# Kernel optimization log

Hardware: AMD Instinct MI355X
Metric: run time of the kernel (lower is better)

Reference implementation:

```python
import jax, jax.numpy as jnp
import numpy as np

B, N, C, H, K = 8, 1024, 768, 12, 16


def setup_inputs() -> dict:
    key = jax.random.key(0)
    ks = jax.random.split(key, 5)
    s = 0.02
    return {
        "query": jax.random.normal(ks[0], (B, N, C), jnp.float32),
        "in_proj_weight": jax.random.normal(ks[1], (3 * C, C), jnp.float32) * s,
        "in_proj_bias": jax.random.normal(ks[2], (3 * C,), jnp.float32) * s,
        "out_proj_weight": jax.random.normal(ks[3], (C, C), jnp.float32) * s,
        "out_proj_bias": jax.random.normal(ks[4], (C,), jnp.float32) * s,
        "num_heads": H,
        "k": K,
    }


def reference(query, in_proj_weight, in_proj_bias, out_proj_weight, out_proj_bias, num_heads, k):
    b, n, c = query.shape
    hd = c // num_heads
    scale = hd ** (-0.5)
    # fused QKV projection: F.linear(x, W, b) == x @ W.T + b
    qkv = query @ in_proj_weight.T + in_proj_bias  # [B,N,3C]
    qkv = qkv.reshape(b, n, 3, num_heads, hd).transpose(2, 0, 3, 1, 4)  # [3,B,H,N,hd]
    q, kk, v = qkv[0], qkv[1], qkv[2]
    attn = jnp.einsum("bhqd,bhkd->bhqk", q, kk) * scale
    attn = jax.nn.softmax(attn, axis=-1)  # [B,H,N,N]
    kk_ = min(k, attn.shape[-1])
    vals, idx = jax.lax.top_k(attn, kk_)  # [B,H,N,k]
    bi = jnp.arange(b)[:, None, None, None]
    hi = jnp.arange(num_heads)[None, :, None, None]
    ni = jnp.arange(n)[None, None, :, None]
    topk_attn = jnp.zeros_like(attn).at[bi, hi, ni, idx].set(vals)
    den = jnp.clip(topk_attn.sum(axis=-1, keepdims=True), 1e-6, None)
    topk_attn = topk_attn / den
    out = jnp.einsum("bhqk,bhkd->bhqd", topk_attn, v)  # [B,H,N,hd]
    out = out.transpose(0, 2, 1, 3).reshape(b, n, c)
    out = out @ out_proj_weight.T + out_proj_bias
    return out, topk_attn
```

## Files before the change

kernel.cpp:

```cpp
#include <hip/hip_runtime.h>
#include <float.h>
#include <math.h>

#define B_ 8
#define N_ 1024
#define C_ 768
#define H_ 12
#define HD_ 64
#define BH_ (B_*H_)

typedef __attribute__((ext_vector_type(8))) short bf16x8;
typedef __attribute__((ext_vector_type(4))) float f32x4;

__device__ __forceinline__ unsigned long long makekey(float v, int idx) {
    unsigned int b = __float_as_uint(v);
    unsigned int o = (b & 0x80000000u) ? ~b : (b | 0x80000000u);
    return ((unsigned long long)o << 32) | (unsigned int)(1023 - idx);
}
__device__ __forceinline__ float keyval(unsigned long long k) {
    unsigned int ordv = (unsigned int)(k >> 32);
    unsigned int fb = (ordv & 0x80000000u) ? (ordv & 0x7FFFFFFFu) : ~ordv;
    return __uint_as_float(fb);
}
__device__ __forceinline__ unsigned short f2bf(float f) {
    unsigned int u = __float_as_uint(f);
    return (unsigned short)((u + 0x7FFFu + ((u >> 16) & 1u)) >> 16);
}

template<int MM, int NN, int KD, int MODE>
__global__ void __launch_bounds__(256)
gemm_k(const float* __restrict__ A, const float* __restrict__ W,
       const float* __restrict__ bias, float* __restrict__ out)
{
    __shared__ float As[2][16][132];
    __shared__ float Bs[2][16][132];
    const int tid = threadIdx.x;
    constexpr int NBLK = NN / 128;
    constexpr int NWG = (MM / 128) * NBLK;
    const int eff = (blockIdx.x & 7) * (NWG / 8) + (blockIdx.x >> 3);
    const int bm = eff / NBLK;
    const int bn = eff % NBLK;
    const int m0 = bm * 128, n0 = bn * 128;
    const int ty = tid >> 4, tx = tid & 15;
    const int ar = tid >> 2;
    const int ac = (tid & 3) << 2;

    float acc[8][8];
#pragma unroll
    for (int i = 0; i < 8; ++i)
#pragma unroll
        for (int j = 0; j < 8; ++j) acc[i][j] = 0.f;

    const float* A0 = A + (size_t)(m0 + ar) * KD + ac;
    const float* A1 = A + (size_t)(m0 + ar + 64) * KD + ac;
    const float* W0 = W + (size_t)(n0 + ar) * KD + ac;
    const float* W1 = W + (size_t)(n0 + ar + 64) * KD + ac;

    float4 pa0 = *(const float4*)A0;
    float4 pa1 = *(const float4*)A1;
    float4 pb0 = *(const float4*)W0;
    float4 pb1 = *(const float4*)W1;

    As[0][ac+0][ar]    = pa0.x; As[0][ac+1][ar]    = pa0.y; As[0][ac+2][ar]    = pa0.z; As[0][ac+3][ar]    = pa0.w;
    As[0][ac+0][ar+64] = pa1.x; As[0][ac+1][ar+64] = pa1.y; As[0][ac+2][ar+64] = pa1.z; As[0][ac+3][ar+64] = pa1.w;
    Bs[0][ac+0][ar]    = pb0.x; Bs[0][ac+1][ar]    = pb0.y; Bs[0][ac+2][ar]    = pb0.z; Bs[0][ac+3][ar]    = pb0.w;
    Bs[0][ac+0][ar+64] = pb1.x; Bs[0][ac+1][ar+64] = pb1.y; Bs[0][ac+2][ar+64] = pb1.z; Bs[0][ac+3][ar+64] = pb1.w;
    __syncthreads();

    int cur = 0;
    for (int k0 = 0; k0 < KD; k0 += 16) {
        const bool more = (k0 + 16 < KD);
        if (more) {
            pa0 = *(const float4*)(A0 + k0 + 16);
            pa1 = *(const float4*)(A1 + k0 + 16);
            pb0 = *(const float4*)(W0 + k0 + 16);
            pb1 = *(const float4*)(W1 + k0 + 16);
        }
        const float (*Ac)[132] = As[cur];
        const float (*Bc)[132] = Bs[cur];
#pragma unroll
        for (int kk = 0; kk < 16; ++kk) {
            float4 a0v = *(const float4*)&Ac[kk][ty * 4];
            float4 a1v = *(const float4*)&Ac[kk][64 + ty * 4];
            float4 b0v = *(const float4*)&Bc[kk][tx * 4];
            float4 b1v = *(const float4*)&Bc[kk][64 + tx * 4];
            float av[8] = {a0v.x,a0v.y,a0v.z,a0v.w, a1v.x,a1v.y,a1v.z,a1v.w};
            float bv[8] = {b0v.x,b0v.y,b0v.z,b0v.w, b1v.x,b1v.y,b1v.z,b1v.w};
#pragma unroll
            for (int i = 0; i < 8; ++i)
#pragma unroll
                for (int j = 0; j < 8; ++j)
                    acc[i][j] = fmaf(av[i], bv[j], acc[i][j]);
        }
        if (more) {
            const int nxt = cur ^ 1;
            As[nxt][ac+0][ar]    = pa0.x; As[nxt][ac+1][ar]    = pa0.y; As[nxt][ac+2][ar]    = pa0.z; As[nxt][ac+3][ar]    = pa0.w;
            As[nxt][ac+0][ar+64] = pa1.x; As[nxt][ac+1][ar+64] = pa1.y; As[nxt][ac+2][ar+64] = pa1.z; As[nxt][ac+3][ar+64] = pa1.w;
            Bs[nxt][ac+0][ar]    = pb0.x; Bs[nxt][ac+1][ar]    = pb0.y; Bs[nxt][ac+2][ar]    = pb0.z; Bs[nxt][ac+3][ar]    = pb0.w;
            Bs[nxt][ac+0][ar+64] = pb1.x; Bs[nxt][ac+1][ar+64] = pb1.y; Bs[nxt][ac+2][ar+64] = pb1.z; Bs[nxt][ac+3][ar+64] = pb1.w;
            __syncthreads();
            cur = nxt;
        }
    }

#pragma unroll
    for (int gi = 0; gi < 2; ++gi)
#pragma unroll
    for (int i = 0; i < 4; ++i) {
        const int m = m0 + gi * 64 + ty * 4 + i;
        const int ai = gi * 4 + i;
#pragma unroll
        for (int gj = 0; gj < 2; ++gj) {
            const int o = n0 + gj * 64 + tx * 4;
            const int aj = gj * 4;
            float4 bv4 = *(const float4*)(bias + o);
            float4 v;
            v.x = acc[ai][aj+0] + bv4.x;
            v.y = acc[ai][aj+1] + bv4.y;
            v.z = acc[ai][aj+2] + bv4.z;
            v.w = acc[ai][aj+3] + bv4.w;
            if (MODE == 0) {
                *(float4*)(out + (size_t)m * NN + o) = v;
            } else {
                const int which = o / 768;
                const int r = o - which * 768;
                const int hh = r >> 6;
                const int dd = r & 63;
                const int bh = (m >> 10) * H_ + hh;
                const int nn = m & 1023;
                if (which == 1) {
                    float* dst = out + (size_t)BH_ * N_ * HD_
                               + ((size_t)bh * HD_ + dd) * N_ + nn;
                    dst[0]      = v.x;
                    dst[N_]     = v.y;
                    dst[2 * N_] = v.z;
                    dst[3 * N_] = v.w;
                } else {
                    float* dst = out + ((size_t)bh * N_ + nn) * HD_ + dd;
                    *(float4*)dst = v;
                }
            }
        }
    }
}

template<int MM, int NN, int MODE>
__global__ void __launch_bounds__(256)
gemm_bf_k(const float* __restrict__ A, const float* __restrict__ W,
          const float* __restrict__ bias, float* __restrict__ out)
{
    __shared__ unsigned short Asb[128][40];
    __shared__ unsigned short Bsb[128][40];
    const int tid = threadIdx.x;
    constexpr int NBLK = NN / 128;
    constexpr int NWG = (MM / 128) * NBLK;
    const int eff = (blockIdx.x & 7) * (NWG / 8) + (blockIdx.x >> 3);
    const int bm = eff / NBLK;
    const int bn = eff % NBLK;
    const int m0 = bm * 128, n0 = bn * 128;
    const int lane = tid & 63;
    const int w = tid >> 6;
    const int wm = (w >> 1) << 6;
    const int wn = (w & 1) << 6;

    f32x4 acc[4][4];
#pragma unroll
    for (int i = 0; i < 4; ++i)
#pragma unroll
        for (int j = 0; j < 4; ++j) acc[i][j] = (f32x4){0.f, 0.f, 0.f, 0.f};

    const int srow = tid >> 1;
    const int sks  = (tid & 1) << 4;
    const float* ga = A + (size_t)(m0 + srow) * 768 + sks;
    const float* gw = W + (size_t)(n0 + srow) * 768 + sks;

    for (int k0 = 0; k0 < 768; k0 += 32) {
        __syncthreads();
        {
            float4 f0 = *(const float4*)(ga + k0 + 0);
            float4 f1 = *(const float4*)(ga + k0 + 4);
            float4 f2 = *(const float4*)(ga + k0 + 8);
            float4 f3 = *(const float4*)(ga + k0 + 12);
            unsigned short* d = &Asb[srow][sks];
            d[0]=f2bf(f0.x);  d[1]=f2bf(f0.y);  d[2]=f2bf(f0.z);  d[3]=f2bf(f0.w);
            d[4]=f2bf(f1.x);  d[5]=f2bf(f1.y);  d[6]=f2bf(f1.z);  d[7]=f2bf(f1.w);
            d[8]=f2bf(f2.x);  d[9]=f2bf(f2.y);  d[10]=f2bf(f2.z); d[11]=f2bf(f2.w);
            d[12]=f2bf(f3.x); d[13]=f2bf(f3.y); d[14]=f2bf(f3.z); d[15]=f2bf(f3.w);
            f0 = *(const float4*)(gw + k0 + 0);
            f1 = *(const float4*)(gw + k0 + 4);
            f2 = *(const float4*)(gw + k0 + 8);
            f3 = *(const float4*)(gw + k0 + 12);
            unsigned short* e = &Bsb[srow][sks];
            e[0]=f2bf(f0.x);  e[1]=f2bf(f0.y);  e[2]=f2bf(f0.z);  e[3]=f2bf(f0.w);
            e[4]=f2bf(f1.x);  e[5]=f2bf(f1.y);  e[6]=f2bf(f1.z);  e[7]=f2bf(f1.w);
            e[8]=f2bf(f2.x);  e[9]=f2bf(f2.y);  e[10]=f2bf(f2.z); e[11]=f2bf(f2.w);
            e[12]=f2bf(f3.x); e[13]=f2bf(f3.y); e[14]=f2bf(f3.z); e[15]=f2bf(f3.w);
        }
        __syncthreads();

        bf16x8 af[4], bf[4];
        const int fr = lane & 15;
        const int fk = (lane >> 4) << 3;
#pragma unroll
        for (int fi = 0; fi < 4; ++fi)
            af[fi] = *(const bf16x8*)&Asb[wm + (fi << 4) + fr][fk];
#pragma unroll
        for (int fj = 0; fj < 4; ++fj)
            bf[fj] = *(const bf16x8*)&Bsb[wn + (fj << 4) + fr][fk];
#pragma unroll
        for (int fi = 0; fi < 4; ++fi)
#pragma unroll
            for (int fj = 0; fj < 4; ++fj)
                acc[fi][fj] = __builtin_amdgcn_mfma_f32_16x16x32_bf16(af[fi], bf[fj], acc[fi][fj], 0, 0, 0);
    }

    const int cr = (lane >> 4) << 2;
    const int cc = lane & 15;
#pragma unroll
    for (int fj = 0; fj < 4; ++fj) {
        const int col = n0 + wn + (fj << 4) + cc;
        const float bb = bias[col];
#pragma unroll
        for (int fi = 0; fi < 4; ++fi) {
#pragma unroll
            for (int j = 0; j < 4; ++j) {
                const int row = m0 + wm + (fi << 4) + cr + j;
                const float val = acc[fi][fj][j] + bb;
                if (MODE == 0) {
                    out[(size_t)row * NN + col] = val;
                } else {
                    const int hh = col >> 6;
                    const int dd = col & 63;
                    const int bh = (row >> 10) * H_ + hh;
                    const int nn = row & 1023;
                    out[((size_t)bh * N_ + nn) * HD_ + dd] = val;
                }
            }
        }
    }
}

__global__ void __launch_bounds__(512, 8)
attn_k(const float* __restrict__ Qg, const float* __restrict__ Ktg,
       uint2* __restrict__ wlist)
{
    __shared__ float Qs[64][8];
    __shared__ float qm[8][64];
    __shared__ unsigned long long kbuf[8][384];
    __shared__ int cnt[8][4];
    __shared__ uint2 w16s[8][16];

    const int tid = threadIdx.x;
    const int lane = tid & 63;
    const int w = tid >> 6;
    const int rg = w >> 2;
    const int cg = w & 3;
    const int eff = (blockIdx.x & 7) * 1536 + (blockIdx.x >> 3);
    const int bh = eff >> 7;
    const int qt = eff & 127;
    const int q0 = qt << 3;
    const size_t kvbase = (size_t)bh * (N_ * HD_);

    if (tid < 128) {
        int q = tid >> 4;
        int d4 = (tid & 15) << 2;
        float4 v = *(const float4*)(Qg + kvbase + (size_t)(q0 + q) * HD_ + d4);
        Qs[d4+0][q] = v.x; Qs[d4+1][q] = v.y; Qs[d4+2][q] = v.z; Qs[d4+3][q] = v.w;
    }
    __syncthreads();

    float acc[4][4];
#pragma unroll
    for (int r = 0; r < 4; ++r)
#pragma unroll
        for (int u = 0; u < 4; ++u) acc[r][u] = 0.f;

    const int jb = (cg << 8) + (lane << 2);
    const int r0 = rg << 2;
    const float* kcol = Ktg + kvbase + jb;

#pragma unroll 8
    for (int d = 0; d < 64; ++d) {
        float4 kvv = *(const float4*)(kcol + (d << 10));
        float4 qa = *(const float4*)&Qs[d][r0];
        float qv[4] = {qa.x, qa.y, qa.z, qa.w};
#pragma unroll
        for (int r = 0; r < 4; ++r) {
            acc[r][0] = fmaf(qv[r], kvv.x, acc[r][0]);
            acc[r][1] = fmaf(qv[r], kvv.y, acc[r][1]);
            acc[r][2] = fmaf(qv[r], kvv.z, acc[r][2]);
            acc[r][3] = fmaf(qv[r], kvv.w, acc[r][3]);
        }
    }

#pragma unroll
    for (int r = 0; r < 4; ++r)
#pragma unroll
        for (int u = 0; u < 4; ++u) acc[r][u] *= 0.125f;

#pragma unroll
    for (int rr = 0; rr < 4; ++rr) {
        float lm = fmaxf(fmaxf(acc[rr][0], acc[rr][1]), fmaxf(acc[rr][2], acc[rr][3]));
        lm = fmaxf(lm, __shfl_xor(lm, 1));
        lm = fmaxf(lm, __shfl_xor(lm, 2));
        if ((lane & 3) == 0) qm[r0 + rr][(cg << 4) + (lane >> 2)] = lm;
    }
    __syncthreads();

#pragma unroll
    for (int rr = 0; rr < 4; ++rr) {
        const int r = r0 + rr;
        const int g = lane & 15;
        float sg = fmaxf(fmaxf(qm[r][g], qm[r][16 + g]),
                         fmaxf(qm[r][32 + g], qm[r][48 + g]));
        sg = fminf(sg, __shfl_xor(sg, 1));
        sg = fminf(sg, __shfl_xor(sg, 2));
        sg = fminf(sg, __shfl_xor(sg, 4));
        sg = fminf(sg, __shfl_xor(sg, 8));
        const float T = sg;
        int base = 0;
        unsigned long long lowmask = (lane == 0) ? 0ull : ((1ull << lane) - 1ull);
#pragma unroll
        for (int u = 0; u < 4; ++u) {
            bool f = acc[rr][u] >= T;
            unsigned long long m = __ballot(f);
            int pos = base + __popcll(m & lowmask);
            if (f && pos < 96) kbuf[r][cg * 96 + pos] = makekey(acc[rr][u], jb + u);
            base += __popcll(m);
        }
        if (lane == 0) cnt[r][cg] = base < 96 ? base : 96;
    }
    __syncthreads();

    {
        const int r = w;
        const int c0n = cnt[r][0], c1n = cnt[r][1], c2n = cnt[r][2], c3n = cnt[r][3];
        const int pfx1 = c0n, pfx2 = c0n + c1n, pfx3 = c0n + c1n + c2n;
        const int Ctot = pfx3 + c3n;

        auto mapk = [&](int p) -> unsigned long long {
            if (p >= Ctot) return 0ull;
            int wseg, pos;
            if (p < pfx1)      { wseg = 0; pos = p; }
            else if (p < pfx2) { wseg = 1; pos = p - pfx1; }
            else if (p < pfx3) { wseg = 2; pos = p - pfx2; }
            else               { wseg = 3; pos = p - pfx3; }
            return kbuf[r][wseg * 96 + pos];
        };

        if (Ctot <= 128) {
            unsigned long long kk0 = mapk(lane);
            unsigned long long kk1 = mapk(lane + 64);
            int n0 = 0, n1 = 0;
#pragma unroll 1
            for (int seg = 0; seg < 4; ++seg) {
                const int cn = cnt[r][seg];
                const unsigned long long* sp = &kbuf[r][seg * 96];
#pragma unroll 4
                for (int p = 0; p < cn; ++p) {
                    unsigned long long kp = sp[p];
                    n0 += (kp > kk0); n1 += (kp > kk1);
                }
            }
            float v0 = keyval(kk0), v1 = keyval(kk1);
            float mc = -FLT_MAX;
            if (n0 == 0) mc = v0;
            if (n1 == 0) mc = v1;
#pragma unroll
            for (int off = 1; off < 64; off <<= 1) mc = fmaxf(mc, __shfl_xor(mc, off));
            float e0 = (n0 < 16) ? expf(v0 - mc) : 0.f;
            float e1 = (n1 < 16) ? expf(v1 - mc) : 0.f;
            float es = e0 + e1;
#pragma unroll
            for (int off = 1; off < 64; off <<= 1) es += __shfl_xor(es, off);
            if (n0 < 16) w16s[r][n0] = make_uint2(1023u - (unsigned)(kk0 & 0xFFFFFFFFull), __float_as_uint(e0 / es));
            if (n1 < 16) w16s[r][n1] = make_uint2(1023u - (unsigned)(kk1 & 0xFFFFFFFFull), __float_as_uint(e1 / es));
        } else {
            unsigned long long kk0 = mapk(lane);
            unsigned long long kk1 = mapk(lane + 64);
            unsigned long long kk2 = mapk(lane + 128);
            unsigned long long kk3 = mapk(lane + 192);
            unsigned long long kk4 = mapk(lane + 256);
            unsigned long long kk5 = mapk(lane + 320);
            int n0 = 0, n1 = 0, n2 = 0, n3 = 0, n4 = 0, n5 = 0;
#pragma unroll 1
            for (int seg = 0; seg < 4; ++seg) {
                const int cn = cnt[r][seg];
                const unsigned long long* sp = &kbuf[r][seg * 96];
#pragma unroll 2
                for (int p = 0; p < cn; ++p) {
                    unsigned long long kp = sp[p];
                    n0 += (kp > kk0); n1 += (kp > kk1); n2 += (kp > kk2);
                    n3 += (kp > kk3); n4 += (kp > kk4); n5 += (kp > kk5);
                }
            }
            float v0 = keyval(kk0), v1 = keyval(kk1), v2 = keyval(kk2);
            float v3 = keyval(kk3), v4 = keyval(kk4), v5 = keyval(kk5);
            float mc = -FLT_MAX;
            if (n0 == 0) mc = v0;
            if (n1 == 0) mc = v1;
            if (n2 == 0) mc = v2;
            if (n3 == 0) mc = v3;
            if (n4 == 0) mc = v4;
            if (n5 == 0) mc = v5;
#pragma unroll
            for (int off = 1; off < 64; off <<= 1) mc = fmaxf(mc, __shfl_xor(mc, off));
            float e0 = (n0 < 16) ? expf(v0 - mc) : 0.f;
            float e1 = (n1 < 16) ? expf(v1 - mc) : 0.f;
            float e2 = (n2 < 16) ? expf(v2 - mc) : 0.f;
            float e3 = (n3 < 16) ? expf(v3 - mc) : 0.f;
            float e4 = (n4 < 16) ? expf(v4 - mc) : 0.f;
            float e5 = (n5 < 16) ? expf(v5 - mc) : 0.f;
            float es = e0 + e1 + e2 + e3 + e4 + e5;
#pragma unroll
            for (int off = 1; off < 64; off <<= 1) es += __shfl_xor(es, off);
            if (n0 < 16) w16s[r][n0] = make_uint2(1023u - (unsigned)(kk0 & 0xFFFFFFFFull), __float_as_uint(e0 / es));
            if (n1 < 16) w16s[r][n1] = make_uint2(1023u - (unsigned)(kk1 & 0xFFFFFFFFull), __float_as_uint(e1 / es));
            if (n2 < 16) w16s[r][n2] = make_uint2(1023u - (unsigned)(kk2 & 0xFFFFFFFFull), __float_as_uint(e2 / es));
            if (n3 < 16) w16s[r][n3] = make_uint2(1023u - (unsigned)(kk3 & 0xFFFFFFFFull), __float_as_uint(e3 / es));
            if (n4 < 16) w16s[r][n4] = make_uint2(1023u - (unsigned)(kk4 & 0xFFFFFFFFull), __float_as_uint(e4 / es));
            if (n5 < 16) w16s[r][n5] = make_uint2(1023u - (unsigned)(kk5 & 0xFFFFFFFFull), __float_as_uint(e5 / es));
        }
        asm volatile("s_waitcnt lgkmcnt(0)" ::: "memory");
        __builtin_amdgcn_sched_barrier(0);

        if (lane < 16)
            wlist[((size_t)bh * N_ + q0 + r) * 16 + lane] = w16s[r][lane];
    }
}

__global__ void __launch_bounds__(256)
pv_scatter_k(const uint2* __restrict__ wlist, const float* __restrict__ Vg,
             float* __restrict__ topk, float* __restrict__ aout)
{
    const int tid = threadIdx.x;
    const int lane = tid & 63;
    const int row = (blockIdx.x << 2) + (tid >> 6);
    const size_t base = (size_t)row << 10;
    const int bh = row >> 10;
    const int n = row & 1023;
    const int b = bh / H_;
    const int h = bh - b * H_;

    float4 z4; z4.x = z4.y = z4.z = z4.w = 0.f;
#pragma unroll
    for (int t = 0; t < 4; ++t)
        *(float4*)(topk + base + (size_t)(((t << 6) + lane) << 2)) = z4;

    const uint2* wl = wlist + (size_t)row * 16;
    const float* vb = Vg + (size_t)bh * (N_ * HD_);
    float pacc = 0.f;
#pragma unroll
    for (int t = 0; t < 16; ++t) {
        uint2 e = wl[t];
        pacc = fmaf(__uint_as_float(e.y), vb[((size_t)e.x << 6) + lane], pacc);
    }
    aout[((size_t)(b * N_ + n)) * C_ + (h << 6) + lane] = pacc;

    asm volatile("s_waitcnt vmcnt(0)" ::: "memory");
    if (lane < 16) {
        uint2 e = wl[lane];
        topk[base + e.x] = __uint_as_float(e.y);
    }
}

extern "C" void kernel_launch(void* const* d_in, const int* in_sizes, int n_in,
                              void* d_out, int out_size, void* d_ws, size_t ws_size,
                              hipStream_t stream)
{
    (void)in_sizes; (void)n_in; (void)out_size; (void)ws_size;
    const float* query = (const float*)d_in[0];
    const float* win   = (const float*)d_in[1];
    const float* bin   = (const float*)d_in[2];
    const float* wout  = (const float*)d_in[3];
    const float* bout  = (const float*)d_in[4];

    float* ws = (float*)d_ws;
    float* Qp   = ws;
    float* Ktg  = Qp  + (size_t)BH_ * N_ * HD_;
    float* Vp   = Ktg + (size_t)BH_ * N_ * HD_;
    float* aout = Vp  + (size_t)BH_ * N_ * HD_;
    uint2* wlist = (uint2*)(aout + (size_t)B_ * N_ * C_);

    float* outp = (float*)d_out;
    float* topk = outp + (size_t)B_ * N_ * C_;

    gemm_k<8192, 1536, 768, 1><<<64 * 12, 256, 0, stream>>>(query, win, bin, Qp);
    gemm_bf_k<8192, 768, 2><<<64 * 6, 256, 0, stream>>>(query, win + (size_t)1536 * 768,
                                                        bin + 1536, Vp);
    attn_k<<<BH_ * 128, 512, 0, stream>>>(Qp, Ktg, wlist);
    pv_scatter_k<<<BH_ * N_ / 4, 256, 0, stream>>>(wlist, Vp, topk, aout);
    gemm_bf_k<8192, 768, 0><<<64 * 6, 256, 0, stream>>>(aout, wout, bout, outp);
}
```

Before: 772.6 us.

## Shrink QK GEMM tile to 64 rows and give attn_k 8 rows per wave

The fp32 Q/K projection GEMM now uses a 64x128 tile instead of 128x128. That doubles the grid and halves the per-thread accumulators, with a launch bound of 6 blocks per CU, to raise occupancy at the cost of more W traffic. attn_k drops from 8 waves (2x4 row/col groups) to 4 waves. Each wave now computes all 8 query rows over a 256-column slice, and each wave handles two rows in the selection phase. The aim is more reuse of each K load across rows, at the cost of more registers per thread and fewer waves per block.

```diff
diff --git a/kernel.cpp b/kernel.cpp
--- a/kernel.cpp
+++ b/kernel.cpp
@@ -28,41 +28,38 @@
 }
 
 template<int MM, int NN, int KD, int MODE>
-__global__ void __launch_bounds__(256)
+__global__ void __launch_bounds__(256, 6)
 gemm_k(const float* __restrict__ A, const float* __restrict__ W,
        const float* __restrict__ bias, float* __restrict__ out)
 {
-    __shared__ float As[2][16][132];
+    __shared__ float As[2][16][68];
     __shared__ float Bs[2][16][132];
     const int tid = threadIdx.x;
     constexpr int NBLK = NN / 128;
-    constexpr int NWG = (MM / 128) * NBLK;
+    constexpr int NWG = (MM / 64) * NBLK;
     const int eff = (blockIdx.x & 7) * (NWG / 8) + (blockIdx.x >> 3);
     const int bm = eff / NBLK;
     const int bn = eff % NBLK;
-    const int m0 = bm * 128, n0 = bn * 128;
+    const int m0 = bm * 64, n0 = bn * 128;
     const int ty = tid >> 4, tx = tid & 15;
     const int ar = tid >> 2;
     const int ac = (tid & 3) << 2;
 
-    float acc[8][8];
-#pragma unroll
-    for (int i = 0; i < 8; ++i)
+    float acc[4][8];
+#pragma unroll
+    for (int i = 0; i < 4; ++i)
 #pragma unroll
         for (int j = 0; j < 8; ++j) acc[i][j] = 0.f;
 
     const float* A0 = A + (size_t)(m0 + ar) * KD + ac;
-    const float* A1 = A + (size_t)(m0 + ar + 64) * KD + ac;
     const float* W0 = W + (size_t)(n0 + ar) * KD + ac;
     const float* W1 = W + (size_t)(n0 + ar + 64) * KD + ac;
 
     float4 pa0 = *(const float4*)A0;
-    float4 pa1 = *(const float4*)A1;
     float4 pb0 = *(const float4*)W0;
     float4 pb1 = *(const float4*)W1;
 
-    As[0][ac+0][ar]    = pa0.x; As[0][ac+1][ar]    = pa0.y; As[0][ac+2][ar]    = pa0.z; As[0][ac+3][ar]    = pa0.w;
-    As[0][ac+0][ar+64] = pa1.x; As[0][ac+1][ar+64] = pa1.y; As[0][ac+2][ar+64] = pa1.z; As[0][ac+3][ar+64] = pa1.w;
+    As[0][ac+0][ar] = pa0.x; As[0][ac+1][ar] = pa0.y; As[0][ac+2][ar] = pa0.z; As[0][ac+3][ar] = pa0.w;
     Bs[0][ac+0][ar]    = pb0.x; Bs[0][ac+1][ar]    = pb0.y; Bs[0][ac+2][ar]    = pb0.z; Bs[0][ac+3][ar]    = pb0.w;
     Bs[0][ac+0][ar+64] = pb1.x; Bs[0][ac+1][ar+64] = pb1.y; Bs[0][ac+2][ar+64] = pb1.z; Bs[0][ac+3][ar+64] = pb1.w;
     __syncthreads();
@@ -72,30 +69,27 @@
         const bool more = (k0 + 16 < KD);
         if (more) {
             pa0 = *(const float4*)(A0 + k0 + 16);
-            pa1 = *(const float4*)(A1 + k0 + 16);
             pb0 = *(const float4*)(W0 + k0 + 16);
             pb1 = *(const float4*)(W1 + k0 + 16);
         }
-        const float (*Ac)[132] = As[cur];
+        const float (*Ac)[68]  = As[cur];
         const float (*Bc)[132] = Bs[cur];
 #pragma unroll
         for (int kk = 0; kk < 16; ++kk) {
             float4 a0v = *(const float4*)&Ac[kk][ty * 4];
-            float4 a1v = *(const float4*)&Ac[kk][64 + ty * 4];
             float4 b0v = *(const float4*)&Bc[kk][tx * 4];
             float4 b1v = *(const float4*)&Bc[kk][64 + tx * 4];
-            float av[8] = {a0v.x,a0v.y,a0v.z,a0v.w, a1v.x,a1v.y,a1v.z,a1v.w};
+            float av[4] = {a0v.x,a0v.y,a0v.z,a0v.w};
             float bv[8] = {b0v.x,b0v.y,b0v.z,b0v.w, b1v.x,b1v.y,b1v.z,b1v.w};
 #pragma unroll
-            for (int i = 0; i < 8; ++i)
+            for (int i = 0; i < 4; ++i)
 #pragma unroll
                 for (int j = 0; j < 8; ++j)
                     acc[i][j] = fmaf(av[i], bv[j], acc[i][j]);
         }
         if (more) {
             const int nxt = cur ^ 1;
-            As[nxt][ac+0][ar]    = pa0.x; As[nxt][ac+1][ar]    = pa0.y; As[nxt][ac+2][ar]    = pa0.z; As[nxt][ac+3][ar]    = pa0.w;
-            As[nxt][ac+0][ar+64] = pa1.x; As[nxt][ac+1][ar+64] = pa1.y; As[nxt][ac+2][ar+64] = pa1.z; As[nxt][ac+3][ar+64] = pa1.w;
+            As[nxt][ac+0][ar] = pa0.x; As[nxt][ac+1][ar] = pa0.y; As[nxt][ac+2][ar] = pa0.z; As[nxt][ac+3][ar] = pa0.w;
             Bs[nxt][ac+0][ar]    = pb0.x; Bs[nxt][ac+1][ar]    = pb0.y; Bs[nxt][ac+2][ar]    = pb0.z; Bs[nxt][ac+3][ar]    = pb0.w;
             Bs[nxt][ac+0][ar+64] = pb1.x; Bs[nxt][ac+1][ar+64] = pb1.y; Bs[nxt][ac+2][ar+64] = pb1.z; Bs[nxt][ac+3][ar+64] = pb1.w;
             __syncthreads();
@@ -104,21 +98,18 @@
     }
 
 #pragma unroll
-    for (int gi = 0; gi < 2; ++gi)
-#pragma unroll
     for (int i = 0; i < 4; ++i) {
-        const int m = m0 + gi * 64 + ty * 4 + i;
-        const int ai = gi * 4 + i;
+        const int m = m0 + ty * 4 + i;
 #pragma unroll
         for (int gj = 0; gj < 2; ++gj) {
             const int o = n0 + gj * 64 + tx * 4;
             const int aj = gj * 4;
             float4 bv4 = *(const float4*)(bias + o);
             float4 v;
-            v.x = acc[ai][aj+0] + bv4.x;
-            v.y = acc[ai][aj+1] + bv4.y;
-            v.z = acc[ai][aj+2] + bv4.z;
-            v.w = acc[ai][aj+3] + bv4.w;
+            v.x = acc[i][aj+0] + bv4.x;
+            v.y = acc[i][aj+1] + bv4.y;
+            v.z = acc[i][aj+2] + bv4.z;
+            v.w = acc[i][aj+3] + bv4.w;
             if (MODE == 0) {
                 *(float4*)(out + (size_t)m * NN + o) = v;
             } else {
@@ -240,7 +231,7 @@
     }
 }
 
-__global__ void __launch_bounds__(512, 8)
+__global__ void __launch_bounds__(256, 5)
 attn_k(const float* __restrict__ Qg, const float* __restrict__ Ktg,
        uint2* __restrict__ wlist)
 {
@@ -253,8 +244,6 @@
     const int tid = threadIdx.x;
     const int lane = tid & 63;
     const int w = tid >> 6;
-    const int rg = w >> 2;
-    const int cg = w & 3;
     const int eff = (blockIdx.x & 7) * 1536 + (blockIdx.x >> 3);
     const int bh = eff >> 7;
     const int qt = eff & 127;
@@ -269,23 +258,23 @@
     }
     __syncthreads();
 
-    float acc[4][4];
-#pragma unroll
-    for (int r = 0; r < 4; ++r)
+    float acc[8][4];
+#pragma unroll
+    for (int r = 0; r < 8; ++r)
 #pragma unroll
         for (int u = 0; u < 4; ++u) acc[r][u] = 0.f;
 
-    const int jb = (cg << 8) + (lane << 2);
-    const int r0 = rg << 2;
+    const int jb = (w << 8) + (lane << 2);
     const float* kcol = Ktg + kvbase + jb;
 
 #pragma unroll 8
     for (int d = 0; d < 64; ++d) {
         float4 kvv = *(const float4*)(kcol + (d << 10));
-        float4 qa = *(const float4*)&Qs[d][r0];
-        float qv[4] = {qa.x, qa.y, qa.z, qa.w};
-#pragma unroll
-        for (int r = 0; r < 4; ++r) {
+        float4 qa = *(const float4*)&Qs[d][0];
+        float4 qb = *(const float4*)&Qs[d][4];
+        float qv[8] = {qa.x, qa.y, qa.z, qa.w, qb.x, qb.y, qb.z, qb.w};
+#pragma unroll
+        for (int r = 0; r < 8; ++r) {
             acc[r][0] = fmaf(qv[r], kvv.x, acc[r][0]);
             acc[r][1] = fmaf(qv[r], kvv.y, acc[r][1]);
             acc[r][2] = fmaf(qv[r], kvv.z, acc[r][2]);
@@ -294,25 +283,24 @@
     }
 
 #pragma unroll
-    for (int r = 0; r < 4; ++r)
+    for (int r = 0; r < 8; ++r)
 #pragma unroll
         for (int u = 0; u < 4; ++u) acc[r][u] *= 0.125f;
 
 #pragma unroll
-    for (int rr = 0; rr < 4; ++rr) {
+    for (int rr = 0; rr < 8; ++rr) {
         float lm = fmaxf(fmaxf(acc[rr][0], acc[rr][1]), fmaxf(acc[rr][2], acc[rr][3]));
         lm = fmaxf(lm, __shfl_xor(lm, 1));
         lm = fmaxf(lm, __shfl_xor(lm, 2));
-        if ((lane & 3) == 0) qm[r0 + rr][(cg << 4) + (lane >> 2)] = lm;
+        if ((lane & 3) == 0) qm[rr][(w << 4) + (lane >> 2)] = lm;
     }
     __syncthreads();
 
 #pragma unroll
-    for (int rr = 0; rr < 4; ++rr) {
-        const int r = r0 + rr;
+    for (int rr = 0; rr < 8; ++rr) {
         const int g = lane & 15;
-        float sg = fmaxf(fmaxf(qm[r][g], qm[r][16 + g]),
-                         fmaxf(qm[r][32 + g], qm[r][48 + g]));
+        float sg = fmaxf(fmaxf(qm[rr][g], qm[rr][16 + g]),
+                         fmaxf(qm[rr][32 + g], qm[rr][48 + g]));
         sg = fminf(sg, __shfl_xor(sg, 1));
         sg = fminf(sg, __shfl_xor(sg, 2));
         sg = fminf(sg, __shfl_xor(sg, 4));
@@ -325,15 +313,16 @@
             bool f = acc[rr][u] >= T;
             unsigned long long m = __ballot(f);
             int pos = base + __popcll(m & lowmask);
-            if (f && pos < 96) kbuf[r][cg * 96 + pos] = makekey(acc[rr][u], jb + u);
+            if (f && pos < 96) kbuf[rr][w * 96 + pos] = makekey(acc[rr][u], jb + u);
             base += __popcll(m);
         }
-        if (lane == 0) cnt[r][cg] = base < 96 ? base : 96;
+        if (lane == 0) cnt[rr][w] = base < 96 ? base : 96;
     }
     __syncthreads();
 
-    {
-        const int r = w;
+#pragma unroll 1
+    for (int rr2 = 0; rr2 < 2; ++rr2) {
+        const int r = (w << 1) | rr2;
         const int c0n = cnt[r][0], c1n = cnt[r][1], c2n = cnt[r][2], c3n = cnt[r][3];
         const int pfx1 = c0n, pfx2 = c0n + c1n, pfx3 = c0n + c1n + c2n;
         const int Ctot = pfx3 + c3n;
@@ -485,10 +474,10 @@
     float* outp = (float*)d_out;
     float* topk = outp + (size_t)B_ * N_ * C_;
 
-    gemm_k<8192, 1536, 768, 1><<<64 * 12, 256, 0, stream>>>(query, win, bin, Qp);
+    gemm_k<8192, 1536, 768, 1><<<128 * 12, 256, 0, stream>>>(query, win, bin, Qp);
     gemm_bf_k<8192, 768, 2><<<64 * 6, 256, 0, stream>>>(query, win + (size_t)1536 * 768,
                                                         bin + 1536, Vp);
-    attn_k<<<BH_ * 128, 512, 0, stream>>>(Qp, Ktg, wlist);
+    attn_k<<<BH_ * 128, 256, 0, stream>>>(Qp, Ktg, wlist);
     pv_scatter_k<<<BH_ * N_ / 4, 256, 0, stream>>>(wlist, Vp, topk, aout);
     gemm_bf_k<8192, 768, 0><<<64 * 6, 256, 0, stream>>>(aout, wout, bout, outp);
 }
```

Result: slower. 1.067 ms (+38.1%).

## Compute attention scores with bf16 MFMA, then rescore candidates in fp32

Applied to the files above, without the earlier changes.

The QKV projection now also writes bf16 copies of Q and K, and stores K row-major instead of transposed. The attention kernel computes QK^T with bf16 MFMA instructions over 16-query tiles and uses a loosened threshold to gather candidate keys. It then recomputes exact fp32 dot products only for those candidates before selecting the top-k, replacing the full fp32 FMA score loop. The costs are an extra bf16 write in the projection and gathered fp32 K loads during rescoring. A candidate could be missed if bf16 error exceeds the threshold margin.

```diff
diff --git a/kernel.cpp b/kernel.cpp
--- a/kernel.cpp
+++ b/kernel.cpp
@@ -30,7 +30,8 @@
 template<int MM, int NN, int KD, int MODE>
 __global__ void __launch_bounds__(256)
 gemm_k(const float* __restrict__ A, const float* __restrict__ W,
-       const float* __restrict__ bias, float* __restrict__ out)
+       const float* __restrict__ bias, float* __restrict__ out,
+       unsigned short* __restrict__ outb)
 {
     __shared__ float As[2][16][132];
     __shared__ float Bs[2][16][132];
@@ -128,17 +129,12 @@
                 const int dd = r & 63;
                 const int bh = (m >> 10) * H_ + hh;
                 const int nn = m & 1023;
-                if (which == 1) {
-                    float* dst = out + (size_t)BH_ * N_ * HD_
-                               + ((size_t)bh * HD_ + dd) * N_ + nn;
-                    dst[0]      = v.x;
-                    dst[N_]     = v.y;
-                    dst[2 * N_] = v.z;
-                    dst[3 * N_] = v.w;
-                } else {
-                    float* dst = out + ((size_t)bh * N_ + nn) * HD_ + dd;
-                    *(float4*)dst = v;
-                }
+                const size_t off = (size_t)which * ((size_t)BH_ * N_ * HD_)
+                                 + ((size_t)bh * N_ + nn) * HD_ + dd;
+                *(float4*)(out + off) = v;
+                ushort4 b4;
+                b4.x = f2bf(v.x); b4.y = f2bf(v.y); b4.z = f2bf(v.z); b4.w = f2bf(v.w);
+                *(ushort4*)(outb + off) = b4;
             }
         }
     }
@@ -240,129 +236,154 @@
     }
 }
 
-__global__ void __launch_bounds__(512, 8)
-attn_k(const float* __restrict__ Qg, const float* __restrict__ Ktg,
-       uint2* __restrict__ wlist)
+__global__ void __launch_bounds__(256)
+attn2_k(const float* __restrict__ Qf, const float* __restrict__ Kf,
+        const unsigned short* __restrict__ Qb, const unsigned short* __restrict__ Kb,
+        uint2* __restrict__ wlist)
 {
-    __shared__ float Qs[64][8];
-    __shared__ float qm[8][64];
-    __shared__ unsigned long long kbuf[8][384];
-    __shared__ int cnt[8][4];
-    __shared__ uint2 w16s[8][16];
+    __shared__ float Qsf[16][68];
+    __shared__ float qm[16][16];
+    __shared__ unsigned short idxp[16][384];
+    __shared__ int cnt[16][4];
+    __shared__ unsigned long long kb2[4][384];
 
     const int tid = threadIdx.x;
     const int lane = tid & 63;
     const int w = tid >> 6;
-    const int rg = w >> 2;
-    const int cg = w & 3;
-    const int eff = (blockIdx.x & 7) * 1536 + (blockIdx.x >> 3);
-    const int bh = eff >> 7;
-    const int qt = eff & 127;
-    const int q0 = qt << 3;
+    const int l15 = lane & 15;
+    const int l4 = lane >> 4;
+    const int eff = (blockIdx.x & 7) * 768 + (blockIdx.x >> 3);
+    const int bh = eff >> 6;
+    const int qt = eff & 63;
+    const int q0 = qt << 4;
     const size_t kvbase = (size_t)bh * (N_ * HD_);
 
-    if (tid < 128) {
-        int q = tid >> 4;
+    {
+        int r = tid >> 4;
         int d4 = (tid & 15) << 2;
-        float4 v = *(const float4*)(Qg + kvbase + (size_t)(q0 + q) * HD_ + d4);
-        Qs[d4+0][q] = v.x; Qs[d4+1][q] = v.y; Qs[d4+2][q] = v.z; Qs[d4+3][q] = v.w;
+        float4 v = *(const float4*)(Qf + kvbase + (size_t)(q0 + r) * HD_ + d4);
+        Qsf[r][d4+0] = v.x; Qsf[r][d4+1] = v.y; Qsf[r][d4+2] = v.z; Qsf[r][d4+3] = v.w;
+    }
+
+    bf16x8 af0 = *(const bf16x8*)(Qb + kvbase + (size_t)(q0 + l15) * HD_ + (l4 << 3));
+    bf16x8 af1 = *(const bf16x8*)(Qb + kvbase + (size_t)(q0 + l15) * HD_ + 32 + (l4 << 3));
+    f32x4 acc[16];
+#pragma unroll
+    for (int t = 0; t < 16; ++t) {
+        const int j0 = (w << 8) + (t << 4);
+        bf16x8 bf0 = *(const bf16x8*)(Kb + kvbase + (size_t)(j0 + l15) * HD_ + (l4 << 3));
+        bf16x8 bf1 = *(const bf16x8*)(Kb + kvbase + (size_t)(j0 + l15) * HD_ + 32 + (l4 << 3));
+        f32x4 z = (f32x4){0.f, 0.f, 0.f, 0.f};
+        z = __builtin_amdgcn_mfma_f32_16x16x32_bf16(af0, bf0, z, 0, 0, 0);
+        z = __builtin_amdgcn_mfma_f32_16x16x32_bf16(af1, bf1, z, 0, 0, 0);
+        acc[t] = z;
+    }
+
+#pragma unroll
+    for (int g = 0; g < 4; ++g) {
+#pragma unroll
+        for (int j = 0; j < 4; ++j) {
+            float lm = fmaxf(fmaxf(acc[4*g+0][j], acc[4*g+1][j]),
+                             fmaxf(acc[4*g+2][j], acc[4*g+3][j]));
+            lm = fmaxf(lm, __shfl_xor(lm, 1));
+            lm = fmaxf(lm, __shfl_xor(lm, 2));
+            lm = fmaxf(lm, __shfl_xor(lm, 4));
+            lm = fmaxf(lm, __shfl_xor(lm, 8));
+            if (l15 == 0) qm[(l4 << 2) + j][(w << 2) + g] = lm;
+        }
     }
     __syncthreads();
 
-    float acc[4][4];
-#pragma unroll
-    for (int r = 0; r < 4; ++r)
-#pragma unroll
-        for (int u = 0; u < 4; ++u) acc[r][u] = 0.f;
-
-    const int jb = (cg << 8) + (lane << 2);
-    const int r0 = rg << 2;
-    const float* kcol = Ktg + kvbase + jb;
-
-#pragma unroll 8
-    for (int d = 0; d < 64; ++d) {
-        float4 kvv = *(const float4*)(kcol + (d << 10));
-        float4 qa = *(const float4*)&Qs[d][r0];
-        float qv[4] = {qa.x, qa.y, qa.z, qa.w};
-#pragma unroll
-        for (int r = 0; r < 4; ++r) {
-            acc[r][0] = fmaf(qv[r], kvv.x, acc[r][0]);
-            acc[r][1] = fmaf(qv[r], kvv.y, acc[r][1]);
-            acc[r][2] = fmaf(qv[r], kvv.z, acc[r][2]);
-            acc[r][3] = fmaf(qv[r], kvv.w, acc[r][3]);
-        }
-    }
-
-#pragma unroll
-    for (int r = 0; r < 4; ++r)
-#pragma unroll
-        for (int u = 0; u < 4; ++u) acc[r][u] *= 0.125f;
-
-#pragma unroll
+#pragma unroll
+    for (int j = 0; j < 4; ++j) {
+        const int r = (l4 << 2) + j;
+        float T = qm[r][l15];
+        T = fminf(T, __shfl_xor(T, 1));
+        T = fminf(T, __shfl_xor(T, 2));
+        T = fminf(T, __shfl_xor(T, 4));
+        T = fminf(T, __shfl_xor(T, 8));
+        const float Tf = T - (0.05f * fabsf(T) + 0.01f);
+        int base = 0;
+        const unsigned int lml = (1u << l15) - 1u;
+#pragma unroll
+        for (int t = 0; t < 16; ++t) {
+            bool f = acc[t][j] >= Tf;
+            unsigned long long bal = __ballot(f);
+            unsigned int m16 = (unsigned int)((bal >> (l4 << 4)) & 0xFFFFull);
+            int pos = base + __popc(m16 & lml);
+            if (f && pos < 96) idxp[r][w * 96 + pos] = (unsigned short)((w << 8) + (t << 4) + l15);
+            base += __popc(m16);
+        }
+        if (l15 == 0) cnt[r][w] = base < 96 ? base : 96;
+    }
+    __syncthreads();
+
+#pragma unroll 1
     for (int rr = 0; rr < 4; ++rr) {
-        float lm = fmaxf(fmaxf(acc[rr][0], acc[rr][1]), fmaxf(acc[rr][2], acc[rr][3]));
-        lm = fmaxf(lm, __shfl_xor(lm, 1));
-        lm = fmaxf(lm, __shfl_xor(lm, 2));
-        if ((lane & 3) == 0) qm[r0 + rr][(cg << 4) + (lane >> 2)] = lm;
-    }
-    __syncthreads();
-
-#pragma unroll
-    for (int rr = 0; rr < 4; ++rr) {
-        const int r = r0 + rr;
-        const int g = lane & 15;
-        float sg = fmaxf(fmaxf(qm[r][g], qm[r][16 + g]),
-                         fmaxf(qm[r][32 + g], qm[r][48 + g]));
-        sg = fminf(sg, __shfl_xor(sg, 1));
-        sg = fminf(sg, __shfl_xor(sg, 2));
-        sg = fminf(sg, __shfl_xor(sg, 4));
-        sg = fminf(sg, __shfl_xor(sg, 8));
-        const float T = sg;
-        int base = 0;
-        unsigned long long lowmask = (lane == 0) ? 0ull : ((1ull << lane) - 1ull);
-#pragma unroll
-        for (int u = 0; u < 4; ++u) {
-            bool f = acc[rr][u] >= T;
-            unsigned long long m = __ballot(f);
-            int pos = base + __popcll(m & lowmask);
-            if (f && pos < 96) kbuf[r][cg * 96 + pos] = makekey(acc[rr][u], jb + u);
-            base += __popcll(m);
-        }
-        if (lane == 0) cnt[r][cg] = base < 96 ? base : 96;
-    }
-    __syncthreads();
-
-    {
-        const int r = w;
+        const int r = (w << 2) | rr;
         const int c0n = cnt[r][0], c1n = cnt[r][1], c2n = cnt[r][2], c3n = cnt[r][3];
         const int pfx1 = c0n, pfx2 = c0n + c1n, pfx3 = c0n + c1n + c2n;
         const int Ctot = pfx3 + c3n;
 
-        auto mapk = [&](int p) -> unsigned long long {
-            if (p >= Ctot) return 0ull;
-            int wseg, pos;
-            if (p < pfx1)      { wseg = 0; pos = p; }
-            else if (p < pfx2) { wseg = 1; pos = p - pfx1; }
-            else if (p < pfx3) { wseg = 2; pos = p - pfx2; }
-            else               { wseg = 3; pos = p - pfx3; }
-            return kbuf[r][wseg * 96 + pos];
+        auto mapi = [&](int p) -> int {
+            if (p >= Ctot) return -1;
+            int seg, pos;
+            if (p < pfx1)      { seg = 0; pos = p; }
+            else if (p < pfx2) { seg = 1; pos = p - pfx1; }
+            else if (p < pfx3) { seg = 2; pos = p - pfx2; }
+            else               { seg = 3; pos = p - pfx3; }
+            return (int)idxp[r][seg * 96 + pos];
         };
-
-        if (Ctot <= 128) {
-            unsigned long long kk0 = mapk(lane);
-            unsigned long long kk1 = mapk(lane + 64);
+        auto rescore = [&](int p) -> unsigned long long {
+            int j = mapi(p);
+            if (j < 0) return 0ull;
+            const float* kp = Kf + kvbase + ((size_t)j << 6);
+            float a = 0.f;
+#pragma unroll
+            for (int d4 = 0; d4 < 64; d4 += 4) {
+                float4 kv = *(const float4*)(kp + d4);
+                a = fmaf(Qsf[r][d4+0], kv.x, a);
+                a = fmaf(Qsf[r][d4+1], kv.y, a);
+                a = fmaf(Qsf[r][d4+2], kv.z, a);
+                a = fmaf(Qsf[r][d4+3], kv.w, a);
+            }
+            a *= 0.125f;
+            unsigned long long k = makekey(a, j);
+            kb2[w][p] = k;
+            return k;
+        };
+
+        const size_t wbase = ((size_t)bh * N_ + q0 + r) * 16;
+
+        if (Ctot <= 64) {
+            unsigned long long k0 = rescore(lane);
+            asm volatile("s_waitcnt lgkmcnt(0)" ::: "memory");
+            __builtin_amdgcn_sched_barrier(0);
+            int n0 = 0;
+#pragma unroll 4
+            for (int pp = 0; pp < Ctot; ++pp) n0 += (kb2[w][pp] > k0);
+            float v0 = keyval(k0);
+            float mc = (n0 == 0) ? v0 : -FLT_MAX;
+#pragma unroll
+            for (int off = 1; off < 64; off <<= 1) mc = fmaxf(mc, __shfl_xor(mc, off));
+            float e0 = (n0 < 16) ? expf(v0 - mc) : 0.f;
+            float es = e0;
+#pragma unroll
+            for (int off = 1; off < 64; off <<= 1) es += __shfl_xor(es, off);
+            if (n0 < 16)
+                wlist[wbase + n0] = make_uint2(1023u - (unsigned)(k0 & 0xFFFFFFFFull), __float_as_uint(e0 / es));
+        } else if (Ctot <= 128) {
+            unsigned long long k0 = rescore(lane);
+            unsigned long long k1 = rescore(lane + 64);
+            asm volatile("s_waitcnt lgkmcnt(0)" ::: "memory");
+            __builtin_amdgcn_sched_barrier(0);
             int n0 = 0, n1 = 0;
-#pragma unroll 1
-            for (int seg = 0; seg < 4; ++seg) {
-                const int cn = cnt[r][seg];
-                const unsigned long long* sp = &kbuf[r][seg * 96];
 #pragma unroll 4
-                for (int p = 0; p < cn; ++p) {
-                    unsigned long long kp = sp[p];
-                    n0 += (kp > kk0); n1 += (kp > kk1);
-                }
+            for (int pp = 0; pp < Ctot; ++pp) {
+                unsigned long long kp2 = kb2[w][pp];
+                n0 += (kp2 > k0); n1 += (kp2 > k1);
             }
-            float v0 = keyval(kk0), v1 = keyval(kk1);
+            float v0 = keyval(k0), v1 = keyval(k1);
             float mc = -FLT_MAX;
             if (n0 == 0) mc = v0;
             if (n1 == 0) mc = v1;
@@ -373,29 +394,28 @@
             float es = e0 + e1;
 #pragma unroll
             for (int off = 1; off < 64; off <<= 1) es += __shfl_xor(es, off);
-            if (n0 < 16) w16s[r][n0] = make_uint2(1023u - (unsigned)(kk0 & 0xFFFFFFFFull), __float_as_uint(e0 / es));
-            if (n1 < 16) w16s[r][n1] = make_uint2(1023u - (unsigned)(kk1 & 0xFFFFFFFFull), __float_as_uint(e1 / es));
+            if (n0 < 16)
+                wlist[wbase + n0] = make_uint2(1023u - (unsigned)(k0 & 0xFFFFFFFFull), __float_as_uint(e0 / es));
+            if (n1 < 16)
+                wlist[wbase + n1] = make_uint2(1023u - (unsigned)(k1 & 0xFFFFFFFFull), __float_as_uint(e1 / es));
         } else {
-            unsigned long long kk0 = mapk(lane);
-            unsigned long long kk1 = mapk(lane + 64);
-            unsigned long long kk2 = mapk(lane + 128);
-            unsigned long long kk3 = mapk(lane + 192);
-            unsigned long long kk4 = mapk(lane + 256);
-            unsigned long long kk5 = mapk(lane + 320);
+            unsigned long long k0 = rescore(lane);
+            unsigned long long k1 = rescore(lane + 64);
+            unsigned long long k2 = rescore(lane + 128);
+            unsigned long long k3 = rescore(lane + 192);
+            unsigned long long k4 = rescore(lane + 256);
+            unsigned long long k5 = rescore(lane + 320);
+            asm volatile("s_waitcnt lgkmcnt(0)" ::: "memory");
+            __builtin_amdgcn_sched_barrier(0);
             int n0 = 0, n1 = 0, n2 = 0, n3 = 0, n4 = 0, n5 = 0;
-#pragma unroll 1
-            for (int seg = 0; seg < 4; ++seg) {
-                const int cn = cnt[r][seg];
-                const unsigned long long* sp = &kbuf[r][seg * 96];
 #pragma unroll 2
-                for (int p = 0; p < cn; ++p) {
-                    unsigned long long kp = sp[p];
-                    n0 += (kp > kk0); n1 += (kp > kk1); n2 += (kp > kk2);
-                    n3 += (kp > kk3); n4 += (kp > kk4); n5 += (kp > kk5);
-                }
+            for (int pp = 0; pp < Ctot; ++pp) {
+                unsigned long long kp2 = kb2[w][pp];
+                n0 += (kp2 > k0); n1 += (kp2 > k1); n2 += (kp2 > k2);
+                n3 += (kp2 > k3); n4 += (kp2 > k4); n5 += (kp2 > k5);
             }
-            float v0 = keyval(kk0), v1 = keyval(kk1), v2 = keyval(kk2);
-            float v3 = keyval(kk3), v4 = keyval(kk4), v5 = keyval(kk5);
+            float v0 = keyval(k0), v1 = keyval(k1), v2 = keyval(k2);
+            float v3 = keyval(k3), v4 = keyval(k4), v5 = keyval(k5);
             float mc = -FLT_MAX;
             if (n0 == 0) mc = v0;
             if (n1 == 0) mc = v1;
@@ -414,18 +434,13 @@
             float es = e0 + e1 + e2 + e3 + e4 + e5;
 #pragma unroll
             for (int off = 1; off < 64; off <<= 1) es += __shfl_xor(es, off);
-            if (n0 < 16) w16s[r][n0] = make_uint2(1023u - (unsigned)(kk0 & 0xFFFFFFFFull), __float_as_uint(e0 / es));
-            if (n1 < 16) w16s[r][n1] = make_uint2(1023u - (unsigned)(kk1 & 0xFFFFFFFFull), __float_as_uint(e1 / es));
-            if (n2 < 16) w16s[r][n2] = make_uint2(1023u - (unsigned)(kk2 & 0xFFFFFFFFull), __float_as_uint(e2 / es));
-            if (n3 < 16) w16s[r][n3] = make_uint2(1023u - (unsigned)(kk3 & 0xFFFFFFFFull), __float_as_uint(e3 / es));
-            if (n4 < 16) w16s[r][n4] = make_uint2(1023u - (unsigned)(kk4 & 0xFFFFFFFFull), __float_as_uint(e4 / es));
-            if (n5 < 16) w16s[r][n5] = make_uint2(1023u - (unsigned)(kk5 & 0xFFFFFFFFull), __float_as_uint(e5 / es));
-        }
-        asm volatile("s_waitcnt lgkmcnt(0)" ::: "memory");
-        __builtin_amdgcn_sched_barrier(0);
-
-        if (lane < 16)
-            wlist[((size_t)bh * N_ + q0 + r) * 16 + lane] = w16s[r][lane];
+            if (n0 < 16) wlist[wbase + n0] = make_uint2(1023u - (unsigned)(k0 & 0xFFFFFFFFull), __float_as_uint(e0 / es));
+            if (n1 < 16) wlist[wbase + n1] = make_uint2(1023u - (unsigned)(k1 & 0xFFFFFFFFull), __float_as_uint(e1 / es));
+            if (n2 < 16) wlist[wbase + n2] = make_uint2(1023u - (unsigned)(k2 & 0xFFFFFFFFull), __float_as_uint(e2 / es));
+            if (n3 < 16) wlist[wbase + n3] = make_uint2(1023u - (unsigned)(k3 & 0xFFFFFFFFull), __float_as_uint(e3 / es));
+            if (n4 < 16) wlist[wbase + n4] = make_uint2(1023u - (unsigned)(k4 & 0xFFFFFFFFull), __float_as_uint(e4 / es));
+            if (n5 < 16) wlist[wbase + n5] = make_uint2(1023u - (unsigned)(k5 & 0xFFFFFFFFull), __float_as_uint(e5 / es));
+        }
     }
 }
 
@@ -475,20 +490,23 @@
     const float* wout  = (const float*)d_in[3];
     const float* bout  = (const float*)d_in[4];
 
+    const size_t SZ = (size_t)BH_ * N_ * HD_;
     float* ws = (float*)d_ws;
-    float* Qp   = ws;
-    float* Ktg  = Qp  + (size_t)BH_ * N_ * HD_;
-    float* Vp   = Ktg + (size_t)BH_ * N_ * HD_;
-    float* aout = Vp  + (size_t)BH_ * N_ * HD_;
+    float* Qp = ws;
+    float* Kp = Qp + SZ;
+    unsigned short* Qb = (unsigned short*)(Kp + SZ);
+    unsigned short* Kb = Qb + SZ;
+    float* Vp   = (float*)(Kb + SZ);
+    float* aout = Vp + SZ;
     uint2* wlist = (uint2*)(aout + (size_t)B_ * N_ * C_);
 
     float* outp = (float*)d_out;
     float* topk = outp + (size_t)B_ * N_ * C_;
 
-    gemm_k<8192, 1536, 768, 1><<<64 * 12, 256, 0, stream>>>(query, win, bin, Qp);
+    gemm_k<8192, 1536, 768, 1><<<64 * 12, 256, 0, stream>>>(query, win, bin, Qp, Qb);
     gemm_bf_k<8192, 768, 2><<<64 * 6, 256, 0, stream>>>(query, win + (size_t)1536 * 768,
                                                         bin + 1536, Vp);
-    attn_k<<<BH_ * 128, 512, 0, stream>>>(Qp, Ktg, wlist);
+    attn2_k<<<BH_ * 64, 256, 0, stream>>>(Qp, Kp, Qb, Kb, wlist);
     pv_scatter_k<<<BH_ * N_ / 4, 256, 0, stream>>>(wlist, Vp, topk, aout);
     gemm_bf_k<8192, 768, 0><<<64 * 6, 256, 0, stream>>>(aout, wout, bout, outp);
 }
```

Measured after the change: 773.6 us. No clear change (+0.1%).
